# Kernel tuning notes

Hardware: AMD Instinct MI355X
Metric: run time of the kernel (lower is better)

## Reference

```python
import jax, jax.numpy as jnp
import numpy as np


def setup_inputs() -> dict:
    key = jax.random.key(0)
    k1, k2, k3, k4 = jax.random.split(key, 4)
    n, C, t, h, w = 1, 256, 8, 64, 64
    heads = 8
    S = t + h + w - 2  # 134 axial positions per query
    attention = jax.random.normal(k1, (n, heads * S, t, h, w), dtype=jnp.float32)
    value = jax.random.normal(k2, (n, C, t, h, w), dtype=jnp.float32)
    conv_w = jax.random.normal(k3, (C, C), dtype=jnp.float32) / np.float32(np.sqrt(C))
    conv_b = jax.random.normal(k4, (C,), dtype=jnp.float32)
    return {"attention": attention, "value": value, "conv_w": conv_w,
            "conv_b": conv_b, "num_heads": heads}


def _grid_attn_map(A, V):
    """Criss-cross axial attention aggregation.
    A: [b, t+h+w-2, t, h, w] per-query weights over the t-axis (t entries,
       self included), h-axis (h-1 entries, self excluded) and w-axis
       (w-1 entries, self excluded).
    V: [b, c, t, h, w]. Returns [b, c, t, h, w].
    """
    b, c, t, h, w = V.shape
    A_t = A[:, :t]                  # [b, t, t, h, w]
    A_h = A[:, t:t + h - 1]         # [b, h-1, t, h, w]
    A_w = A[:, t + h - 1:]          # [b, w-1, t, h, w]

    # t-axis (self included): sum over key frame s
    out = jnp.einsum('bsthw,bcshw->bcthw', A_t, V)

    # h-axis (self excluded): channel j addresses key row p = j + (j >= q).
    # Build dense [h] channel axis with a zero at p == q via a padded gather.
    zpad = jnp.zeros((b, 1, t, h, w), A.dtype)
    A_h_pad = jnp.concatenate([A_h, zpad], axis=1)  # channel h-1 is zero
    p = jnp.arange(h)[:, None]
    q = jnp.arange(h)[None, :]
    inv_h = jnp.where(p < q, p, jnp.where(p == q, h - 1, p - 1))  # [h(p), h(q)]
    A_h_full = jnp.take_along_axis(A_h_pad, inv_h[None, :, None, :, None], axis=1)  # [b,p,t,q,w]
    out = out + jnp.einsum('bptqw,bctpw->bctqw', A_h_full, V)

    # w-axis (self excluded), same trick along w
    A_w_pad = jnp.concatenate([A_w, zpad], axis=1)  # channel w-1 is zero (h==w here OK; recompute pad generally)
    pw = jnp.arange(w)[:, None]
    qw = jnp.arange(w)[None, :]
    inv_w = jnp.where(pw < qw, pw, jnp.where(pw == qw, w - 1, pw - 1))  # [w(p), w(q)]
    A_w_full = jnp.take_along_axis(A_w_pad, inv_w[None, :, None, None, :], axis=1)  # [b,p,t,h,q]
    out = out + jnp.einsum('bpthq,bcthp->bcthq', A_w_full, V)
    return out


def reference(attention, value, conv_w, conv_b, num_heads):
    n, C, t, h, w = value.shape
    S = t + h + w - 2
    # 1x1x1 Conv3d == per-position channel matmul
    pv = jnp.einsum('ncthw,oc->nothw', value, conv_w) + conv_b[None, :, None, None, None]
    pv = pv.reshape(n * num_heads, C // num_heads, t, h, w)
    A = attention.reshape(n * num_heads, S, t, h, w)
    out = _grid_attn_map(A, pv)
    return out.reshape(n, num_heads, C // num_heads, t, h, w)
```

## Files before the change

kernel.cpp:

```cpp
#include <hip/hip_runtime.h>

#define SS   134
#define HWP  4096
#define THW  32768

typedef float f32x4 __attribute__((ext_vector_type(4)));
typedef short bf16x8 __attribute__((ext_vector_type(8)));
typedef short bf16x4 __attribute__((ext_vector_type(4)));

__device__ __forceinline__ float vget(const float4& v, int j) {
  return j == 0 ? v.x : j == 1 ? v.y : j == 2 ? v.z : v.w;
}

__device__ __forceinline__ unsigned short f2bf(float f) {
  unsigned int u = __float_as_uint(f);
  u += 0x7fff + ((u >> 16) & 1);
  return (unsigned short)(u >> 16);
}

__global__ __launch_bounds__(256, 4) void conv1x1_mfma(
    const float* __restrict__ V, const float* __restrict__ W,
    const float* __restrict__ bias, float* __restrict__ PV) {
  __shared__ unsigned short sW[256 * 40];
  __shared__ unsigned short sV[32 * 40];
  const int tid = threadIdx.x;
  const int x0 = blockIdx.x * 32;
  const int lane = tid & 63;
  const int wv = tid >> 6;
  const int m = lane & 15;
  const int q = lane >> 4;

  f32x4 acc[4][2];
#pragma unroll
  for (int i = 0; i < 4; ++i)
#pragma unroll
    for (int j = 0; j < 2; ++j)
      acc[i][j] = (f32x4){0.f, 0.f, 0.f, 0.f};

  for (int k0 = 0; k0 < 256; k0 += 32) {
#pragma unroll
    for (int r = 0; r < 8; ++r) {
      const int f = r * 256 + tid;
      const int o = f >> 3;
      const int c4 = (f & 7) * 4;
      const float4 w4 = *(const float4*)&W[o * 256 + k0 + c4];
      bf16x4 b;
      b.x = (short)f2bf(w4.x);
      b.y = (short)f2bf(w4.y);
      b.z = (short)f2bf(w4.z);
      b.w = (short)f2bf(w4.w);
      *(bf16x4*)&sW[o * 40 + c4] = b;
    }
    {
      const int c = tid >> 3;
      const int x4 = (tid & 7) * 4;
      const float4 v4 = *(const float4*)&V[(size_t)(k0 + c) * THW + x0 + x4];
      sV[(x4 + 0) * 40 + c] = f2bf(v4.x);
      sV[(x4 + 1) * 40 + c] = f2bf(v4.y);
      sV[(x4 + 2) * 40 + c] = f2bf(v4.z);
      sV[(x4 + 3) * 40 + c] = f2bf(v4.w);
    }
    __syncthreads();
    bf16x8 fa[4], fb[2];
#pragma unroll
    for (int i = 0; i < 4; ++i)
      fa[i] = *(const bf16x8*)&sW[(wv * 64 + i * 16 + m) * 40 + q * 8];
#pragma unroll
    for (int j = 0; j < 2; ++j)
      fb[j] = *(const bf16x8*)&sV[(j * 16 + m) * 40 + q * 8];
#pragma unroll
    for (int i = 0; i < 4; ++i)
#pragma unroll
      for (int j = 0; j < 2; ++j)
        acc[i][j] = __builtin_amdgcn_mfma_f32_16x16x32_bf16(fa[i], fb[j], acc[i][j], 0, 0, 0);
    __syncthreads();
  }

#pragma unroll
  for (int i = 0; i < 4; ++i) {
#pragma unroll
    for (int r = 0; r < 4; ++r) {
      const int o = wv * 64 + i * 16 + q * 4 + r;
      const float b = bias[o];
#pragma unroll
      for (int j = 0; j < 2; ++j)
        PV[(size_t)o * THW + x0 + j * 16 + m] = acc[i][j][r] + b;
    }
  }
}

__global__ __launch_bounds__(256, 8) void grid_attn_kernel(
    const float* __restrict__ A, const float* __restrict__ PV,
    float* __restrict__ O) {
  const int blk = blockIdx.x;
  const int hq0 = (blk & 31) * 2;
  const int tq = (blk >> 5) & 7;
  const int hd = blk >> 8;
  const int tid = threadIdx.x;
  const int wq4 = (tid & 15) * 4;
  const int c0 = tid >> 4;

  const float* __restrict__ Ab = A + (size_t)hd * SS * THW + (size_t)tq * HWP;
  const float* __restrict__ PVh = PV + (size_t)hd * 32 * THW;
  float* __restrict__ Oh = O + (size_t)hd * 32 * THW;

  __shared__ float sPVw[32 * 2 * 68];

  {
    const int c = tid >> 3;
    const int q = (tid >> 2) & 1;
    const int p0 = (tid & 3) * 16;
    const float* src = &PVh[(size_t)c * THW + (size_t)tq * HWP + (hq0 + q) * 64 + p0];
    float* dst = &sPVw[(c * 2 + q) * 68 + p0];
#pragma unroll
    for (int i = 0; i < 4; ++i)
      *(float4*)(dst + i * 4) = *(const float4*)(src + i * 4);
  }
  __syncthreads();

  float acc[2][2][4] = {};

#pragma unroll
  for (int s = 0; s < 8; ++s) {
#pragma unroll
    for (int q = 0; q < 2; ++q) {
      const int hq = hq0 + q;
      const float4 a = *(const float4*)&Ab[(size_t)s * THW + hq * 64 + wq4];
      const float4 v0 = *(const float4*)&PVh[(size_t)c0 * THW + (size_t)s * HWP + hq * 64 + wq4];
      const float4 v1 = *(const float4*)&PVh[(size_t)(c0 + 16) * THW + (size_t)s * HWP + hq * 64 + wq4];
#pragma unroll
      for (int j = 0; j < 4; ++j) {
        acc[0][q][j] += vget(a, j) * vget(v0, j);
        acc[1][q][j] += vget(a, j) * vget(v1, j);
      }
    }
  }

#pragma unroll 2
  for (int p = 0; p < 64; ++p) {
    const float4 v0 = *(const float4*)&PVh[(size_t)c0 * THW + (size_t)tq * HWP + p * 64 + wq4];
    const float4 v1 = *(const float4*)&PVh[(size_t)(c0 + 16) * THW + (size_t)tq * HWP + p * 64 + wq4];
#pragma unroll
    for (int q = 0; q < 2; ++q) {
      const int hq = hq0 + q;
      const int idx = (p < hq) ? p : (p > 0 ? p - 1 : 0);
      const float msk = (p == hq) ? 0.f : 1.f;
      const float4 a = *(const float4*)&Ab[(size_t)(8 + idx) * THW + hq * 64 + wq4];
#pragma unroll
      for (int j = 0; j < 4; ++j) {
        const float w = vget(a, j) * msk;
        acc[0][q][j] += w * vget(v0, j);
        acc[1][q][j] += w * vget(v1, j);
      }
    }
  }

  float cur[2][2], nxt[2][2];
#pragma unroll
  for (int q = 0; q < 2; ++q) {
    cur[0][q] = sPVw[(c0 * 2 + q) * 68];
    cur[1][q] = sPVw[((c0 + 16) * 2 + q) * 68];
  }
  for (int r = 0; r < 63; ++r) {
#pragma unroll
    for (int q = 0; q < 2; ++q) {
      nxt[0][q] = sPVw[(c0 * 2 + q) * 68 + r + 1];
      nxt[1][q] = sPVw[((c0 + 16) * 2 + q) * 68 + r + 1];
    }
#pragma unroll
    for (int q = 0; q < 2; ++q) {
      const int hq = hq0 + q;
      const float4 a = *(const float4*)&Ab[(size_t)(71 + r) * THW + hq * 64 + wq4];
#pragma unroll
      for (int j = 0; j < 4; ++j) {
        const float w = vget(a, j);
        const bool lt = (r < wq4 + j);
        acc[0][q][j] += w * (lt ? cur[0][q] : nxt[0][q]);
        acc[1][q][j] += w * (lt ? cur[1][q] : nxt[1][q]);
      }
    }
#pragma unroll
    for (int q = 0; q < 2; ++q) {
      cur[0][q] = nxt[0][q];
      cur[1][q] = nxt[1][q];
    }
  }

#pragma unroll
  for (int ch = 0; ch < 2; ++ch) {
    const int c = ch ? (c0 + 16) : c0;
#pragma unroll
    for (int q = 0; q < 2; ++q) {
      float4 r;
      r.x = acc[ch][q][0];
      r.y = acc[ch][q][1];
      r.z = acc[ch][q][2];
      r.w = acc[ch][q][3];
      *(float4*)&Oh[(size_t)c * THW + (size_t)tq * HWP + (hq0 + q) * 64 + wq4] = r;
    }
  }
}

extern "C" void kernel_launch(void* const* d_in, const int* in_sizes, int n_in,
                              void* d_out, int out_size, void* d_ws, size_t ws_size,
                              hipStream_t stream) {
  const float* A = (const float*)d_in[0];
  const float* V = (const float*)d_in[1];
  const float* W = (const float*)d_in[2];
  const float* bias = (const float*)d_in[3];
  float* out = (float*)d_out;
  float* pv = (float*)d_ws;

  conv1x1_mfma<<<dim3(1024), 256, 0, stream>>>(V, W, bias, pv);
  grid_attn_kernel<<<dim3(2048), 256, 0, stream>>>(A, pv, out);
}
```

Measured before the change: 392.6 us.

## Restructure grid attention: 512-thread blocks, one channel per thread, split h-loop at diagonal

The grid attention kernel now uses 512 threads per block with one channel per thread instead of two. Block order is remapped so tq and head vary fastest. The h-axis loop is split around the diagonal, which removes the per-iteration index select and mask multiply, and both the h and w loops are unrolled by 4 with batched loads. The conv kernel drops its occupancy hint and partially unrolls the weight staging loop. The aim is less index arithmetic and more memory-level parallelism. The cost is that each attention weight load is shared by half as many channels per thread, so more per-thread load instructions.

```diff
diff --git a/kernel.cpp b/kernel.cpp
--- a/kernel.cpp
+++ b/kernel.cpp
@@ -18,7 +18,7 @@
   return (unsigned short)(u >> 16);
 }
 
-__global__ __launch_bounds__(256, 4) void conv1x1_mfma(
+__global__ __launch_bounds__(256) void conv1x1_v2(
     const float* __restrict__ V, const float* __restrict__ W,
     const float* __restrict__ bias, float* __restrict__ PV) {
   __shared__ unsigned short sW[256 * 40];
@@ -38,7 +38,7 @@
       acc[i][j] = (f32x4){0.f, 0.f, 0.f, 0.f};
 
   for (int k0 = 0; k0 < 256; k0 += 32) {
-#pragma unroll
+#pragma unroll 2
     for (int r = 0; r < 8; ++r) {
       const int f = r * 256 + tid;
       const int o = f >> 3;
@@ -89,115 +89,184 @@
   }
 }
 
-__global__ __launch_bounds__(256, 8) void grid_attn_kernel(
+__global__ __launch_bounds__(512, 4) void grid_attn_v2(
     const float* __restrict__ A, const float* __restrict__ PV,
     float* __restrict__ O) {
   const int blk = blockIdx.x;
-  const int hq0 = (blk & 31) * 2;
-  const int tq = (blk >> 5) & 7;
-  const int hd = blk >> 8;
+  const int tq = blk & 7;
+  const int hd = (blk >> 3) & 7;
+  const int hq0 = (blk >> 6) * 2;
   const int tid = threadIdx.x;
   const int wq4 = (tid & 15) * 4;
-  const int c0 = tid >> 4;
+  const int c = tid >> 4;
 
   const float* __restrict__ Ab = A + (size_t)hd * SS * THW + (size_t)tq * HWP;
-  const float* __restrict__ PVh = PV + (size_t)hd * 32 * THW;
-  float* __restrict__ Oh = O + (size_t)hd * 32 * THW;
+  const float* __restrict__ PVc = PV + (size_t)(hd * 32 + c) * THW;
 
   __shared__ float sPVw[32 * 2 * 68];
 
+#pragma unroll
+  for (int i = 0; i < 2; ++i) {
+    const int fid = tid + i * 512;
+    const int cq = fid >> 4;
+    const int p4 = (fid & 15) * 4;
+    const float* src = &PV[(size_t)(hd * 32 + (cq >> 1)) * THW + (size_t)tq * HWP +
+                           (hq0 + (cq & 1)) * 64 + p4];
+    *(float4*)&sPVw[cq * 68 + p4] = *(const float4*)src;
+  }
+  __syncthreads();
+
+  float acc[2][4] = {};
+
+#pragma unroll
+  for (int s = 0; s < 8; ++s) {
+#pragma unroll
+    for (int q = 0; q < 2; ++q) {
+      const float4 a = *(const float4*)&Ab[(size_t)s * THW + (hq0 + q) * 64 + wq4];
+      const float4 v = *(const float4*)&PVc[(size_t)s * HWP + (hq0 + q) * 64 + wq4];
+#pragma unroll
+      for (int j = 0; j < 4; ++j) acc[q][j] += vget(a, j) * vget(v, j);
+    }
+  }
+
   {
-    const int c = tid >> 3;
-    const int q = (tid >> 2) & 1;
-    const int p0 = (tid & 3) * 16;
-    const float* src = &PVh[(size_t)c * THW + (size_t)tq * HWP + (hq0 + q) * 64 + p0];
-    float* dst = &sPVw[(c * 2 + q) * 68 + p0];
-#pragma unroll
-    for (int i = 0; i < 4; ++i)
-      *(float4*)(dst + i * 4) = *(const float4*)(src + i * 4);
-  }
-  __syncthreads();
-
-  float acc[2][2][4] = {};
-
-#pragma unroll
-  for (int s = 0; s < 8; ++s) {
-#pragma unroll
-    for (int q = 0; q < 2; ++q) {
-      const int hq = hq0 + q;
-      const float4 a = *(const float4*)&Ab[(size_t)s * THW + hq * 64 + wq4];
-      const float4 v0 = *(const float4*)&PVh[(size_t)c0 * THW + (size_t)s * HWP + hq * 64 + wq4];
-      const float4 v1 = *(const float4*)&PVh[(size_t)(c0 + 16) * THW + (size_t)s * HWP + hq * 64 + wq4];
+    const float* pA0 = Ab + (size_t)8 * THW + hq0 * 64 + wq4;
+    const float* pA1 = pA0 + 64;
+    const float* pV = PVc + (size_t)tq * HWP + wq4;
+
+    int p = 0;
+    for (; p + 4 <= hq0; p += 4) {
+      float4 a0[4], a1[4], vv[4];
+#pragma unroll
+      for (int u = 0; u < 4; ++u) {
+        a0[u] = *(const float4*)(pA0 + (size_t)u * THW);
+        a1[u] = *(const float4*)(pA1 + (size_t)u * THW);
+        vv[u] = *(const float4*)(pV + (size_t)(p + u) * 64);
+      }
+#pragma unroll
+      for (int u = 0; u < 4; ++u)
+#pragma unroll
+        for (int j = 0; j < 4; ++j) {
+          acc[0][j] += vget(a0[u], j) * vget(vv[u], j);
+          acc[1][j] += vget(a1[u], j) * vget(vv[u], j);
+        }
+      pA0 += 4 * (size_t)THW;
+      pA1 += 4 * (size_t)THW;
+    }
+    for (; p < hq0; ++p) {
+      const float4 a0 = *(const float4*)pA0;
+      const float4 a1 = *(const float4*)pA1;
+      const float4 vv = *(const float4*)(pV + (size_t)p * 64);
 #pragma unroll
       for (int j = 0; j < 4; ++j) {
-        acc[0][q][j] += vget(a, j) * vget(v0, j);
-        acc[1][q][j] += vget(a, j) * vget(v1, j);
-      }
-    }
-  }
-
-#pragma unroll 2
-  for (int p = 0; p < 64; ++p) {
-    const float4 v0 = *(const float4*)&PVh[(size_t)c0 * THW + (size_t)tq * HWP + p * 64 + wq4];
-    const float4 v1 = *(const float4*)&PVh[(size_t)(c0 + 16) * THW + (size_t)tq * HWP + p * 64 + wq4];
-#pragma unroll
-    for (int q = 0; q < 2; ++q) {
-      const int hq = hq0 + q;
-      const int idx = (p < hq) ? p : (p > 0 ? p - 1 : 0);
-      const float msk = (p == hq) ? 0.f : 1.f;
-      const float4 a = *(const float4*)&Ab[(size_t)(8 + idx) * THW + hq * 64 + wq4];
+        acc[0][j] += vget(a0, j) * vget(vv, j);
+        acc[1][j] += vget(a1, j) * vget(vv, j);
+      }
+      pA0 += THW;
+      pA1 += THW;
+    }
+    {
+      const float4 a1 = *(const float4*)pA1;
+      const float4 vv = *(const float4*)(pV + (size_t)hq0 * 64);
+#pragma unroll
+      for (int j = 0; j < 4; ++j) acc[1][j] += vget(a1, j) * vget(vv, j);
+      pA1 += THW;
+    }
+    {
+      const float4 a0 = *(const float4*)pA0;
+      const float4 vv = *(const float4*)(pV + (size_t)(hq0 + 1) * 64);
+#pragma unroll
+      for (int j = 0; j < 4; ++j) acc[0][j] += vget(a0, j) * vget(vv, j);
+      pA0 += THW;
+    }
+    p = hq0 + 2;
+    for (; p + 4 <= 64; p += 4) {
+      float4 a0[4], a1[4], vv[4];
+#pragma unroll
+      for (int u = 0; u < 4; ++u) {
+        a0[u] = *(const float4*)(pA0 + (size_t)u * THW);
+        a1[u] = *(const float4*)(pA1 + (size_t)u * THW);
+        vv[u] = *(const float4*)(pV + (size_t)(p + u) * 64);
+      }
+#pragma unroll
+      for (int u = 0; u < 4; ++u)
+#pragma unroll
+        for (int j = 0; j < 4; ++j) {
+          acc[0][j] += vget(a0[u], j) * vget(vv[u], j);
+          acc[1][j] += vget(a1[u], j) * vget(vv[u], j);
+        }
+      pA0 += 4 * (size_t)THW;
+      pA1 += 4 * (size_t)THW;
+    }
+    for (; p < 64; ++p) {
+      const float4 a0 = *(const float4*)pA0;
+      const float4 a1 = *(const float4*)pA1;
+      const float4 vv = *(const float4*)(pV + (size_t)p * 64);
 #pragma unroll
       for (int j = 0; j < 4; ++j) {
-        const float w = vget(a, j) * msk;
-        acc[0][q][j] += w * vget(v0, j);
-        acc[1][q][j] += w * vget(v1, j);
-      }
-    }
-  }
-
-  float cur[2][2], nxt[2][2];
+        acc[0][j] += vget(a0, j) * vget(vv, j);
+        acc[1][j] += vget(a1, j) * vget(vv, j);
+      }
+      pA0 += THW;
+      pA1 += THW;
+    }
+  }
+
+  {
+    const int base0 = (c * 2 + 0) * 68;
+    const int base1 = (c * 2 + 1) * 68;
+    float cur0 = sPVw[base0];
+    float cur1 = sPVw[base1];
+    const float* pAw = Ab + (size_t)71 * THW + hq0 * 64 + wq4;
+    int r = 0;
+    for (; r + 4 <= 63; r += 4) {
+      float4 a0[4], a1[4];
+#pragma unroll
+      for (int u = 0; u < 4; ++u) {
+        a0[u] = *(const float4*)(pAw + (size_t)u * THW);
+        a1[u] = *(const float4*)(pAw + (size_t)u * THW + 64);
+      }
+#pragma unroll
+      for (int u = 0; u < 4; ++u) {
+        const int rr = r + u;
+        const float nxt0 = sPVw[base0 + rr + 1];
+        const float nxt1 = sPVw[base1 + rr + 1];
+#pragma unroll
+        for (int j = 0; j < 4; ++j) {
+          const bool lt = (rr < wq4 + j);
+          acc[0][j] += vget(a0[u], j) * (lt ? cur0 : nxt0);
+          acc[1][j] += vget(a1[u], j) * (lt ? cur1 : nxt1);
+        }
+        cur0 = nxt0;
+        cur1 = nxt1;
+      }
+      pAw += 4 * (size_t)THW;
+    }
+    for (; r < 63; ++r) {
+      const float4 a0 = *(const float4*)pAw;
+      const float4 a1 = *(const float4*)(pAw + 64);
+      const float nxt0 = sPVw[base0 + r + 1];
+      const float nxt1 = sPVw[base1 + r + 1];
+#pragma unroll
+      for (int j = 0; j < 4; ++j) {
+        const bool lt = (r < wq4 + j);
+        acc[0][j] += vget(a0, j) * (lt ? cur0 : nxt0);
+        acc[1][j] += vget(a1, j) * (lt ? cur1 : nxt1);
+      }
+      cur0 = nxt0;
+      cur1 = nxt1;
+      pAw += THW;
+    }
+  }
+
 #pragma unroll
   for (int q = 0; q < 2; ++q) {
-    cur[0][q] = sPVw[(c0 * 2 + q) * 68];
-    cur[1][q] = sPVw[((c0 + 16) * 2 + q) * 68];
-  }
-  for (int r = 0; r < 63; ++r) {
-#pragma unroll
-    for (int q = 0; q < 2; ++q) {
-      nxt[0][q] = sPVw[(c0 * 2 + q) * 68 + r + 1];
-      nxt[1][q] = sPVw[((c0 + 16) * 2 + q) * 68 + r + 1];
-    }
-#pragma unroll
-    for (int q = 0; q < 2; ++q) {
-      const int hq = hq0 + q;
-      const float4 a = *(const float4*)&Ab[(size_t)(71 + r) * THW + hq * 64 + wq4];
-#pragma unroll
-      for (int j = 0; j < 4; ++j) {
-        const float w = vget(a, j);
-        const bool lt = (r < wq4 + j);
-        acc[0][q][j] += w * (lt ? cur[0][q] : nxt[0][q]);
-        acc[1][q][j] += w * (lt ? cur[1][q] : nxt[1][q]);
-      }
-    }
-#pragma unroll
-    for (int q = 0; q < 2; ++q) {
-      cur[0][q] = nxt[0][q];
-      cur[1][q] = nxt[1][q];
-    }
-  }
-
-#pragma unroll
-  for (int ch = 0; ch < 2; ++ch) {
-    const int c = ch ? (c0 + 16) : c0;
-#pragma unroll
-    for (int q = 0; q < 2; ++q) {
-      float4 r;
-      r.x = acc[ch][q][0];
-      r.y = acc[ch][q][1];
-      r.z = acc[ch][q][2];
-      r.w = acc[ch][q][3];
-      *(float4*)&Oh[(size_t)c * THW + (size_t)tq * HWP + (hq0 + q) * 64 + wq4] = r;
-    }
+    float4 r;
+    r.x = acc[q][0];
+    r.y = acc[q][1];
+    r.z = acc[q][2];
+    r.w = acc[q][3];
+    *(float4*)&O[(size_t)(hd * 32 + c) * THW + (size_t)tq * HWP + (hq0 + q) * 64 + wq4] = r;
   }
 }
 
@@ -211,6 +280,6 @@
   float* out = (float*)d_out;
   float* pv = (float*)d_ws;
 
-  conv1x1_mfma<<<dim3(1024), 256, 0, stream>>>(V, W, bias, pv);
-  grid_attn_kernel<<<dim3(2048), 256, 0, stream>>>(A, pv, out);
-}
+  conv1x1_v2<<<dim3(1024), 256, 0, stream>>>(V, W, bias, pv);
+  grid_attn_v2<<<dim3(2048), 512, 0, stream>>>(A, pv, out);
+}
```

Result: slower. 445.8 us (+13.5%).

## Split grid attention into t+h and w kernels with register tiling over queries and channels

Applied to the files above, without the earlier changes.

The fused attention kernel is replaced by two kernels. The first handles the t and h axes with 4x4 register tiles over query rows and channels, and caches a PV slab in LDS. The second handles the w axis with a transposed LDS slab and accumulates into the output written by the first kernel. The aim is more reuse of each attention and PV load per FMA, in exchange for an extra kernel launch and an extra read-modify-write of the output. Launch bounds and unroll hints on the conv kernel are also loosened.

```diff
diff --git a/kernel.cpp b/kernel.cpp
--- a/kernel.cpp
+++ b/kernel.cpp
@@ -7,10 +7,6 @@
 typedef float f32x4 __attribute__((ext_vector_type(4)));
 typedef short bf16x8 __attribute__((ext_vector_type(8)));
 typedef short bf16x4 __attribute__((ext_vector_type(4)));
-
-__device__ __forceinline__ float vget(const float4& v, int j) {
-  return j == 0 ? v.x : j == 1 ? v.y : j == 2 ? v.z : v.w;
-}
 
 __device__ __forceinline__ unsigned short f2bf(float f) {
   unsigned int u = __float_as_uint(f);
@@ -18,7 +14,7 @@
   return (unsigned short)(u >> 16);
 }
 
-__global__ __launch_bounds__(256, 4) void conv1x1_mfma(
+__global__ __launch_bounds__(256) void conv1x1_v2(
     const float* __restrict__ V, const float* __restrict__ W,
     const float* __restrict__ bias, float* __restrict__ PV) {
   __shared__ unsigned short sW[256 * 40];
@@ -38,7 +34,7 @@
       acc[i][j] = (f32x4){0.f, 0.f, 0.f, 0.f};
 
   for (int k0 = 0; k0 < 256; k0 += 32) {
-#pragma unroll
+#pragma unroll 2
     for (int r = 0; r < 8; ++r) {
       const int f = r * 256 + tid;
       const int o = f >> 3;
@@ -89,115 +85,157 @@
   }
 }
 
-__global__ __launch_bounds__(256, 8) void grid_attn_kernel(
+__global__ __launch_bounds__(256) void attn_th(
     const float* __restrict__ A, const float* __restrict__ PV,
     float* __restrict__ O) {
-  const int blk = blockIdx.x;
-  const int hq0 = (blk & 31) * 2;
-  const int tq = (blk >> 5) & 7;
-  const int hd = blk >> 8;
+  const int b = blockIdx.x;
+  const int wb = b & 7;
+  const int tq = (b >> 3) & 7;
+  const int hd = b >> 6;
   const int tid = threadIdx.x;
-  const int wq4 = (tid & 15) * 4;
-  const int c0 = tid >> 4;
+  const int w4 = (tid & 1) * 4;
+  const int q16 = (tid >> 1) & 15;
+  const int cg = tid >> 5;
+
+  __shared__ float slab[32 * 64 * 8];
 
   const float* __restrict__ Ab = A + (size_t)hd * SS * THW + (size_t)tq * HWP;
-  const float* __restrict__ PVh = PV + (size_t)hd * 32 * THW;
-  float* __restrict__ Oh = O + (size_t)hd * 32 * THW;
-
-  __shared__ float sPVw[32 * 2 * 68];
-
-  {
-    const int c = tid >> 3;
-    const int q = (tid >> 2) & 1;
-    const int p0 = (tid & 3) * 16;
-    const float* src = &PVh[(size_t)c * THW + (size_t)tq * HWP + (hq0 + q) * 64 + p0];
-    float* dst = &sPVw[(c * 2 + q) * 68 + p0];
-#pragma unroll
-    for (int i = 0; i < 4; ++i)
-      *(float4*)(dst + i * 4) = *(const float4*)(src + i * 4);
+  const size_t pvh = (size_t)hd * 32 * THW;
+
+#pragma unroll 4
+  for (int i = 0; i < 16; ++i) {
+    const int fid = tid + i * 256;
+    const int ws = (fid & 1) * 4;
+    const int p = (fid >> 1) & 63;
+    const int c = fid >> 7;
+    *(f32x4*)&slab[(c * 64 + p) * 8 + ws] =
+        *(const f32x4*)&PV[pvh + (size_t)c * THW + (size_t)tq * HWP + p * 64 + wb * 8 + ws];
   }
   __syncthreads();
 
-  float acc[2][2][4] = {};
-
-#pragma unroll
+  f32x4 acc[4][4];
+#pragma unroll
+  for (int i = 0; i < 4; ++i)
+#pragma unroll
+    for (int j = 0; j < 4; ++j)
+      acc[i][j] = (f32x4){0.f, 0.f, 0.f, 0.f};
+
   for (int s = 0; s < 8; ++s) {
 #pragma unroll
-    for (int q = 0; q < 2; ++q) {
-      const int hq = hq0 + q;
-      const float4 a = *(const float4*)&Ab[(size_t)s * THW + hq * 64 + wq4];
-      const float4 v0 = *(const float4*)&PVh[(size_t)c0 * THW + (size_t)s * HWP + hq * 64 + wq4];
-      const float4 v1 = *(const float4*)&PVh[(size_t)(c0 + 16) * THW + (size_t)s * HWP + hq * 64 + wq4];
-#pragma unroll
-      for (int j = 0; j < 4; ++j) {
-        acc[0][q][j] += vget(a, j) * vget(v0, j);
-        acc[1][q][j] += vget(a, j) * vget(v1, j);
+    for (int qq = 0; qq < 4; ++qq) {
+      const int q = qq * 16 + q16;
+      const f32x4 a = *(const f32x4*)&Ab[(size_t)s * THW + q * 64 + wb * 8 + w4];
+#pragma unroll
+      for (int ci = 0; ci < 4; ++ci) {
+        const int c = cg + ci * 8;
+        const f32x4 v =
+            *(const f32x4*)&PV[pvh + (size_t)c * THW + (size_t)s * HWP + q * 64 + wb * 8 + w4];
+        acc[qq][ci] += a * v;
       }
     }
   }
 
+  const float* __restrict__ Ah = Ab + (size_t)8 * THW + wb * 8 + w4;
 #pragma unroll 2
   for (int p = 0; p < 64; ++p) {
-    const float4 v0 = *(const float4*)&PVh[(size_t)c0 * THW + (size_t)tq * HWP + p * 64 + wq4];
-    const float4 v1 = *(const float4*)&PVh[(size_t)(c0 + 16) * THW + (size_t)tq * HWP + p * 64 + wq4];
-#pragma unroll
-    for (int q = 0; q < 2; ++q) {
-      const int hq = hq0 + q;
-      const int idx = (p < hq) ? p : (p > 0 ? p - 1 : 0);
-      const float msk = (p == hq) ? 0.f : 1.f;
-      const float4 a = *(const float4*)&Ab[(size_t)(8 + idx) * THW + hq * 64 + wq4];
-#pragma unroll
-      for (int j = 0; j < 4; ++j) {
-        const float w = vget(a, j) * msk;
-        acc[0][q][j] += w * vget(v0, j);
-        acc[1][q][j] += w * vget(v1, j);
-      }
-    }
-  }
-
-  float cur[2][2], nxt[2][2];
-#pragma unroll
-  for (int q = 0; q < 2; ++q) {
-    cur[0][q] = sPVw[(c0 * 2 + q) * 68];
-    cur[1][q] = sPVw[((c0 + 16) * 2 + q) * 68];
-  }
-  for (int r = 0; r < 63; ++r) {
-#pragma unroll
-    for (int q = 0; q < 2; ++q) {
-      nxt[0][q] = sPVw[(c0 * 2 + q) * 68 + r + 1];
-      nxt[1][q] = sPVw[((c0 + 16) * 2 + q) * 68 + r + 1];
-    }
-#pragma unroll
-    for (int q = 0; q < 2; ++q) {
-      const int hq = hq0 + q;
-      const float4 a = *(const float4*)&Ab[(size_t)(71 + r) * THW + hq * 64 + wq4];
-#pragma unroll
-      for (int j = 0; j < 4; ++j) {
-        const float w = vget(a, j);
-        const bool lt = (r < wq4 + j);
-        acc[0][q][j] += w * (lt ? cur[0][q] : nxt[0][q]);
-        acc[1][q][j] += w * (lt ? cur[1][q] : nxt[1][q]);
-      }
-    }
-#pragma unroll
-    for (int q = 0; q < 2; ++q) {
-      cur[0][q] = nxt[0][q];
-      cur[1][q] = nxt[1][q];
-    }
-  }
-
-#pragma unroll
-  for (int ch = 0; ch < 2; ++ch) {
-    const int c = ch ? (c0 + 16) : c0;
-#pragma unroll
-    for (int q = 0; q < 2; ++q) {
-      float4 r;
-      r.x = acc[ch][q][0];
-      r.y = acc[ch][q][1];
-      r.z = acc[ch][q][2];
-      r.w = acc[ch][q][3];
-      *(float4*)&Oh[(size_t)c * THW + (size_t)tq * HWP + (hq0 + q) * 64 + wq4] = r;
-    }
+    f32x4 av[4];
+#pragma unroll
+    for (int qq = 0; qq < 4; ++qq) {
+      const int q = qq * 16 + q16;
+      const int row = p - (q < p ? 1 : 0);
+      f32x4 a = *(const f32x4*)&Ah[(size_t)row * THW + q * 64];
+      if (q == p) a = (f32x4){0.f, 0.f, 0.f, 0.f};
+      av[qq] = a;
+    }
+    f32x4 vv[4];
+#pragma unroll
+    for (int ci = 0; ci < 4; ++ci)
+      vv[ci] = *(const f32x4*)&slab[((cg + ci * 8) * 64 + p) * 8 + w4];
+#pragma unroll
+    for (int qq = 0; qq < 4; ++qq)
+#pragma unroll
+      for (int ci = 0; ci < 4; ++ci)
+        acc[qq][ci] += av[qq] * vv[ci];
+  }
+
+#pragma unroll
+  for (int qq = 0; qq < 4; ++qq) {
+    const int q = qq * 16 + q16;
+#pragma unroll
+    for (int ci = 0; ci < 4; ++ci) {
+      const int c = cg + ci * 8;
+      *(f32x4*)&O[pvh + (size_t)c * THW + (size_t)tq * HWP + q * 64 + wb * 8 + w4] =
+          acc[qq][ci];
+    }
+  }
+}
+
+__global__ __launch_bounds__(256) void attn_w(
+    const float* __restrict__ A, const float* __restrict__ PV,
+    float* __restrict__ O) {
+  const int b = blockIdx.x;
+  const int hb = b & 15;
+  const int tq = (b >> 4) & 7;
+  const int hd = b >> 7;
+  const int tid = threadIdx.x;
+  const int wq = tid & 63;
+  const int cg = tid >> 6;
+  const int h0 = hb * 4;
+
+  __shared__ float slab[32 * 64 * 4];
+
+  const float* __restrict__ Ab = A + (size_t)hd * SS * THW + (size_t)tq * HWP;
+  const size_t pvh = (size_t)hd * 32 * THW;
+
+#pragma unroll 4
+  for (int i = 0; i < 8; ++i) {
+    const int fid = tid + i * 256;
+    const int w4s = (fid & 15) * 4;
+    const int h = (fid >> 4) & 3;
+    const int c = fid >> 6;
+    const f32x4 v =
+        *(const f32x4*)&PV[pvh + (size_t)c * THW + (size_t)tq * HWP + (h0 + h) * 64 + w4s];
+    slab[(c * 64 + w4s + 0) * 4 + h] = v.x;
+    slab[(c * 64 + w4s + 1) * 4 + h] = v.y;
+    slab[(c * 64 + w4s + 2) * 4 + h] = v.z;
+    slab[(c * 64 + w4s + 3) * 4 + h] = v.w;
+  }
+
+  f32x4 racc[8];
+#pragma unroll
+  for (int ci = 0; ci < 8; ++ci) {
+    const int c = cg + ci * 4;
+    f32x4 r;
+#pragma unroll
+    for (int hh = 0; hh < 4; ++hh)
+      r[hh] = O[pvh + (size_t)c * THW + (size_t)tq * HWP + (h0 + hh) * 64 + wq];
+    racc[ci] = r;
+  }
+  __syncthreads();
+
+#pragma unroll 2
+  for (int p = 0; p < 64; ++p) {
+    const int row = 71 + p - (wq <= p ? 1 : 0);
+    const float* pa = Ab + (size_t)row * THW + h0 * 64 + wq;
+    f32x4 a;
+    a.x = pa[0];
+    a.y = pa[64];
+    a.z = pa[128];
+    a.w = pa[192];
+    if (p == wq) a = (f32x4){0.f, 0.f, 0.f, 0.f};
+#pragma unroll
+    for (int ci = 0; ci < 8; ++ci) {
+      const f32x4 v = *(const f32x4*)&slab[(cg + ci * 4) * 256 + p * 4];
+      racc[ci] += a * v;
+    }
+  }
+
+#pragma unroll
+  for (int ci = 0; ci < 8; ++ci) {
+    const int c = cg + ci * 4;
+#pragma unroll
+    for (int hh = 0; hh < 4; ++hh)
+      O[pvh + (size_t)c * THW + (size_t)tq * HWP + (h0 + hh) * 64 + wq] = racc[ci][hh];
   }
 }
 
@@ -211,6 +249,7 @@
   float* out = (float*)d_out;
   float* pv = (float*)d_ws;
 
-  conv1x1_mfma<<<dim3(1024), 256, 0, stream>>>(V, W, bias, pv);
-  grid_attn_kernel<<<dim3(2048), 256, 0, stream>>>(A, pv, out);
-}
+  conv1x1_v2<<<dim3(1024), 256, 0, stream>>>(V, W, bias, pv);
+  attn_th<<<dim3(512), 256, 0, stream>>>(A, pv, out);
+  attn_w<<<dim3(1024), 256, 0, stream>>>(A, pv, out);
+}
```

Result: faster. 380.1 us (-3.2%).
